# Optimization experiments

Measured on AMD Instinct MI355X. Metric: run time of the kernel, lower is better.

Reference implementation:

```python
import jax, jax.numpy as jnp
import numpy as np

DELTA_V = 0.1
DELTA_D = 0.5
NUM_LABELS = 33  # label 0 = background, instance ids 1..32


def setup_inputs() -> dict:
    key = jax.random.key(0)
    k1, k2 = jax.random.split(key)
    B, N, D = 8, 131072, 32
    embeddings = jax.random.normal(k1, (B, N, D), dtype=jnp.float32)
    labels = jax.random.randint(k2, (B, N), 0, NUM_LABELS, dtype=jnp.int32)
    return {"embeddings": embeddings, "labels": labels}


def reference(embeddings, labels):
    # embeddings: [B, N, D], labels: [B, N] int (0 = ignore)
    B = embeddings.shape[0]
    dt = embeddings.dtype

    oh = jax.nn.one_hot(labels, NUM_LABELS, dtype=dt)              # [B, N, L]
    counts = oh.sum(1)                                              # [B, L]
    sums = jnp.einsum('bnl,bnd->bld', oh, embeddings)               # [B, L, D]
    means = sums / jnp.maximum(counts, 1.0)[..., None]              # [B, L, D]

    # ---- pull loss: hinge on distance of each point to its instance mean ----
    mean_pt = jnp.take_along_axis(means, labels[..., None], axis=1)  # [B, N, D]
    diff = embeddings - mean_pt
    dist = jnp.sqrt(jnp.sum(diff * diff, -1) + 1e-24)               # [B, N]
    hinge = jnp.maximum(dist - DELTA_V, 0.0)
    seg_mean = jnp.einsum('bnl,bn->bl', oh, hinge) / jnp.maximum(counts, 1.0)  # [B, L]

    present = counts[:, 1:] > 0                                     # [B, L-1]
    n_inst = present.sum(-1).astype(dt)                             # [B]
    pull_b = seg_mean[:, 1:].sum(-1) / (n_inst + 1e-6)
    pull = pull_b.sum() / B

    # ---- push loss: hinge margin between normalized instance means ----
    m = means[:, 1:, :]                                             # [B, L-1, D]
    mn = m / jnp.maximum(jnp.linalg.norm(m, axis=-1, keepdims=True), 1e-12)
    sq = jnp.sum((mn[:, :, None, :] - mn[:, None, :, :]) ** 2, -1)  # [B, K, K]
    dmat = jnp.sqrt(sq + 1e-24)
    K = NUM_LABELS - 1
    triu = jnp.triu(jnp.ones((K, K), dt), 1)
    pmask = triu[None] * present[:, :, None].astype(dt) * present[:, None, :].astype(dt)
    hp = jnp.maximum(2.0 * DELTA_D - dmat, 0.0) * pmask
    push_b = jnp.where(n_inst > 1, hp.sum((-2, -1)) / (pmask.sum((-2, -1)) + 1e-6), 0.0)
    push = push_b.sum() / B

    total = pull + push
    return jnp.stack([total, pull, push])
```

## Files before the change

### kernel.cpp

```cpp
#include <hip/hip_runtime.h>
#include <hip/hip_bf16.h>

#define BATCH 8
#define NPTS  131072
#define DIM   32
#define NLAB  33
#define G1X   256
#define P1PTS 512
#define BPB2  128

#define OFF_CNT   0
#define OFF_SUM   264
#define OFF_PULL  (264 + 8448)
#define WS_FLOATS (OFF_PULL + BATCH * BPB2)

typedef short  bf16x8 __attribute__((ext_vector_type(8)));
typedef float  f32x4  __attribute__((ext_vector_type(4)));

static __device__ __forceinline__ short f2bf(float f) {
  __hip_bfloat16 h = __float2bfloat16(f);
  return *reinterpret_cast<short*>(&h);
}

__global__ __launch_bounds__(256) void pass1_kernel(
    const float* __restrict__ emb, const int* __restrict__ lab,
    float* __restrict__ gsum, float* __restrict__ gcnt) {
  const int b    = blockIdx.y;
  const int tid  = threadIdx.x;
  const int w    = tid >> 6;
  const int lane = tid & 63;

  constexpr int STEPS = P1PTS / 128;

  __shared__ float s_stage[4][32 * 33];
  __shared__ int   s_cnt4[4][NLAB];
  float* st = s_stage[w];

  const size_t base = (size_t)b * NPTS + (size_t)blockIdx.x * P1PTS
                    + (size_t)w * (P1PTS / 4);

  const int m0 = lane & 15;
  const int g  = lane >> 4;
  f32x4 acc[3][2];
#pragma unroll
  for (int t = 0; t < 3; ++t)
#pragma unroll
    for (int u = 0; u < 2; ++u) acc[t][u] = (f32x4){0.f, 0.f, 0.f, 0.f};
  int cnt0 = 0, cnt1 = 0, cnt2 = 0;

  float4 ld[4];
  int labv;
  {
    const float4* src = (const float4*)(emb + base * DIM);
#pragma unroll
    for (int r = 0; r < 4; ++r) ld[r] = src[lane + 64 * r];
    labv = lab[base + (lane & 31)];
  }

  for (int step = 0; step < STEPS; ++step) {
#pragma unroll
    for (int r = 0; r < 4; ++r) {
      const int i = lane + 64 * r;
      const int p = i >> 3, d0 = (i & 7) * 4;
      st[(d0 + 0) * 33 + p] = ld[r].x;
      st[(d0 + 1) * 33 + p] = ld[r].y;
      st[(d0 + 2) * 33 + p] = ld[r].z;
      st[(d0 + 3) * 33 + p] = ld[r].w;
    }
    const int labv_c = labv;

    if (step < STEPS - 1) {
      const float4* src = (const float4*)(emb + (base + (step + 1) * 32) * DIM);
#pragma unroll
      for (int r = 0; r < 4; ++r) ld[r] = src[lane + 64 * r];
      labv = lab[base + (step + 1) * 32 + (lane & 31)];
    }

    bf16x8 a0, a1, a2;
#pragma unroll
    for (int j = 0; j < 8; ++j) {
      const int lj = __shfl(labv_c, g * 8 + j);
      const int h0 = (lj == m0), h1 = (lj == m0 + 16), h2 = (lj == m0 + 32);
      a0[j] = h0 ? (short)0x3F80 : (short)0;
      a1[j] = h1 ? (short)0x3F80 : (short)0;
      a2[j] = h2 ? (short)0x3F80 : (short)0;
      cnt0 += h0; cnt1 += h1; cnt2 += h2;
    }

    bf16x8 b0, b1;
#pragma unroll
    for (int j = 0; j < 8; ++j) {
      b0[j] = f2bf(st[m0 * 33 + g * 8 + j]);
      b1[j] = f2bf(st[(m0 + 16) * 33 + g * 8 + j]);
    }

    acc[0][0] = __builtin_amdgcn_mfma_f32_16x16x32_bf16(a0, b0, acc[0][0], 0, 0, 0);
    acc[0][1] = __builtin_amdgcn_mfma_f32_16x16x32_bf16(a0, b1, acc[0][1], 0, 0, 0);
    acc[1][0] = __builtin_amdgcn_mfma_f32_16x16x32_bf16(a1, b0, acc[1][0], 0, 0, 0);
    acc[1][1] = __builtin_amdgcn_mfma_f32_16x16x32_bf16(a1, b1, acc[1][1], 0, 0, 0);
    acc[2][0] = __builtin_amdgcn_mfma_f32_16x16x32_bf16(a2, b0, acc[2][0], 0, 0, 0);
    acc[2][1] = __builtin_amdgcn_mfma_f32_16x16x32_bf16(a2, b1, acc[2][1], 0, 0, 0);
  }

  cnt0 += __shfl_xor(cnt0, 16); cnt0 += __shfl_xor(cnt0, 32);
  cnt1 += __shfl_xor(cnt1, 16); cnt1 += __shfl_xor(cnt1, 32);
  cnt2 += __shfl_xor(cnt2, 16); cnt2 += __shfl_xor(cnt2, 32);
  if (lane < 16)            s_cnt4[w][m0]      = cnt0;
  else if (lane < 32)       s_cnt4[w][m0 + 16] = cnt1;
  if (lane == 32)           s_cnt4[w][32]      = cnt2;

#pragma unroll
  for (int t = 0; t < 2; ++t)
#pragma unroll
    for (int u = 0; u < 2; ++u)
#pragma unroll
      for (int r = 0; r < 4; ++r)
        st[(t * 16 + g * 4 + r) * DIM + m0 + 16 * u] = acc[t][u][r];
  if (lane < 16) {
    st[32 * DIM + m0]      = acc[2][0][0];
    st[32 * DIM + m0 + 16] = acc[2][1][0];
  }
  __syncthreads();

  for (int i = tid; i < NLAB * DIM; i += 256) {
    const float v = s_stage[0][i] + s_stage[1][i] + s_stage[2][i] + s_stage[3][i];
    atomicAdd(&gsum[(size_t)b * (NLAB * DIM) + i], v);
  }
  if (tid < NLAB) {
    const int c = s_cnt4[0][tid] + s_cnt4[1][tid] + s_cnt4[2][tid] + s_cnt4[3][tid];
    atomicAdd(&gcnt[b * NLAB + tid], (float)c);
  }
}

#define CN 8
#define P2_ISSUE(LB, EB, C)                                                   \
  {                                                                           \
    _Pragma("unroll")                                                         \
    for (int j = 0; j < CN; ++j) {                                            \
      const size_t it = (size_t)(C) * CN + j;                                 \
      const unsigned long long al =                                           \
          (unsigned long long)(lab + base + p0 + it * PSTRIDE);               \
      asm volatile("global_load_dword %0, %1, off" : "=&v"(LB[j]) : "v"(al)); \
    }                                                                         \
    _Pragma("unroll")                                                         \
    for (int j = 0; j < CN; ++j) {                                            \
      const size_t it = (size_t)(C) * CN + j;                                 \
      const unsigned long long ae =                                           \
          (unsigned long long)(emb + (base + p0 + it * PSTRIDE) * DIM + d0);  \
      asm volatile("global_load_dwordx4 %0, %1, off" : "=&v"(EB[j]) : "v"(ae)); \
    }                                                                         \
  }

#define P2_COMPUTE(LB, EB)                                                    \
  {                                                                           \
    float s[CN];                                                              \
    _Pragma("unroll")                                                         \
    for (int j = 0; j < CN; ++j) {                                            \
      const f32x4 mv = *(const f32x4*)(s_mean + LB[j] * 36 + d0);             \
      const float dx = EB[j][0] - mv[0], dy = EB[j][1] - mv[1];               \
      const float dz = EB[j][2] - mv[2], dw = EB[j][3] - mv[3];               \
      s[j] = dx * dx + dy * dy + dz * dz + dw * dw;                           \
    }                                                                         \
    _Pragma("unroll")                                                         \
    for (int j = 0; j < CN; ++j) {                                            \
      s[j] += __shfl_xor(s[j], 1);                                            \
      s[j] += __shfl_xor(s[j], 2);                                            \
      s[j] += __shfl_xor(s[j], 4);                                            \
    }                                                                         \
    float sv = s[0];                                                          \
    int   lv = LB[0];                                                         \
    _Pragma("unroll")                                                         \
    for (int j = 1; j < CN; ++j) {                                            \
      sv = (lane8 == j) ? s[j] : sv;                                          \
      lv = (lane8 == j) ? LB[j] : lv;                                         \
    }                                                                         \
    const float dist = sqrtf(sv + 1e-24f);                                    \
    wacc += s_w[lv] * fmaxf(dist - 0.1f, 0.f);                                \
  }

__global__ __launch_bounds__(256, 4) void pass2_kernel(
    const float* __restrict__ emb, const int* __restrict__ lab,
    const float* __restrict__ gsum, const float* __restrict__ gcnt,
    float* __restrict__ pull_part) {
  const int b   = blockIdx.y;
  const int tid = threadIdx.x;
  __shared__ __align__(16) float s_mean[NLAB * 36];
  __shared__ float s_w[NLAB];
  __shared__ float s_red[4];

  for (int i = tid; i < NLAB * DIM; i += 256) {
    const int l = i >> 5, d = i & 31;
    const float c = gcnt[b * NLAB + l];
    s_mean[l * 36 + d] = gsum[b * (NLAB * DIM) + i] / fmaxf(c, 1.0f);
  }
  if (tid < 64) {
    const float c = (tid < NLAB) ? gcnt[b * NLAB + tid] : 0.f;
    const int pres = (tid >= 1 && tid < NLAB && c > 0.f) ? 1 : 0;
    const unsigned long long bal = __ballot(pres);
    const float n_inst = (float)__popcll(bal);
    if (tid < NLAB)
      s_w[tid] = pres ? 1.f / (fmaxf(c, 1.f) * (n_inst + 1e-6f)) : 0.f;
  }
  __syncthreads();

  const int sub   = tid >> 3;
  const int lane8 = tid & 7;
  const int d0    = lane8 << 2;
  const size_t base = (size_t)b * NPTS;
  const int p0 = blockIdx.x * 32 + sub;
  constexpr int PSTRIDE = BPB2 * 32;
  constexpr int NIT     = NPTS / PSTRIDE;
  constexpr int NCH     = NIT / CN;

  int   labsA[CN], labsB[CN];
  f32x4 eA[CN], eB[CN];
  float wacc = 0.f;

  P2_ISSUE(labsA, eA, 0);
#pragma unroll
  for (int cc = 0; cc < NCH; cc += 2) {
    if (cc + 1 < NCH) P2_ISSUE(labsB, eB, cc + 1);
    if (cc + 1 < NCH) { asm volatile("s_waitcnt vmcnt(16)" ::: "memory"); }
    else              { asm volatile("s_waitcnt vmcnt(0)"  ::: "memory"); }
    __builtin_amdgcn_sched_barrier(0);
    P2_COMPUTE(labsA, eA);
    if (cc + 1 < NCH) {
      if (cc + 2 < NCH) P2_ISSUE(labsA, eA, cc + 2);
      if (cc + 2 < NCH) { asm volatile("s_waitcnt vmcnt(16)" ::: "memory"); }
      else              { asm volatile("s_waitcnt vmcnt(0)"  ::: "memory"); }
      __builtin_amdgcn_sched_barrier(0);
      P2_COMPUTE(labsB, eB);
    }
  }

#pragma unroll
  for (int mm = 1; mm < 64; mm <<= 1) wacc += __shfl_xor(wacc, mm);
  if ((tid & 63) == 0) s_red[tid >> 6] = wacc;
  __syncthreads();
  if (tid == 0)
    pull_part[b * BPB2 + blockIdx.x] =
        s_red[0] + s_red[1] + s_red[2] + s_red[3];
}

__global__ __launch_bounds__(512) void finish_kernel(
    const float* __restrict__ gsum, const float* __restrict__ gcnt,
    const float* __restrict__ pull_part, float* __restrict__ out) {
  const int tid = threadIdx.x;
  const int b   = tid >> 6;
  const int t   = tid & 63;
  __shared__ __align__(16) float s_mn[BATCH * 32 * DIM];
  __shared__ float s_ps[BATCH];
  __shared__ float s_pl[BATCH];
  float* mn = s_mn + b * 32 * DIM;

  {
    float plsum = pull_part[b * BPB2 + t] + pull_part[b * BPB2 + 64 + t];
#pragma unroll
    for (int m = 1; m < 64; m <<= 1) plsum += __shfl_xor(plsum, m);
    if (t == 0) s_pl[b] = plsum;
  }

  int pres = 0;
  if (t < 32) {
    const int l = t + 1;
    const float cnt = gcnt[b * NLAB + l];
    pres = (cnt > 0.f) ? 1 : 0;
    const float inv = 1.f / fmaxf(cnt, 1.f);
    float v[DIM];
    float n2 = 0.f;
    for (int d = 0; d < DIM; d++) {
      v[d] = gsum[b * (NLAB * DIM) + l * DIM + d] * inv;
      n2  += v[d] * v[d];
    }
    const float scale = 1.f / fmaxf(sqrtf(n2), 1e-12f);
    for (int d = 0; d < DIM; d++) mn[t * DIM + d] = v[d] * scale;
  }
  const unsigned long long bal = __ballot(pres);
  const unsigned int pmask32 = (unsigned int)(bal & 0xFFFFFFFFull);
  const int n_inst = __popc(pmask32);

  __syncthreads();

  float hp_sum = 0.f, pm_sum = 0.f;
  for (int idx = t; idx < 1024; idx += 64) {
    const int i = idx >> 5, j = idx & 31;
    if (j > i && ((pmask32 >> i) & 1u) && ((pmask32 >> j) & 1u)) {
      const float4* a = (const float4*)(mn + i * DIM);
      const float4* c = (const float4*)(mn + j * DIM);
      float sq = 0.f;
      for (int q = 0; q < 8; q++) {
        const float4 av = a[q], cv = c[q];
        const float dx = av.x - cv.x, dy = av.y - cv.y;
        const float dz = av.z - cv.z, dw = av.w - cv.w;
        sq += dx * dx + dy * dy + dz * dz + dw * dw;
      }
      const float dmat = sqrtf(sq + 1e-24f);
      hp_sum += fmaxf(1.0f - dmat, 0.f);
      pm_sum += 1.f;
    }
  }
  for (int m = 1; m < 64; m <<= 1) {
    hp_sum += __shfl_xor(hp_sum, m);
    pm_sum += __shfl_xor(pm_sum, m);
  }
  const float push = (n_inst > 1) ? hp_sum / (pm_sum + 1e-6f) : 0.f;
  if (t == 0) s_ps[b] = push;
  __syncthreads();

  if (tid < 64) {
    float pl = (t < BATCH) ? s_pl[t] : 0.f;
    float ps = (t < BATCH) ? s_ps[t] : 0.f;
#pragma unroll
    for (int m = 1; m < 64; m <<= 1) {
      pl += __shfl_xor(pl, m);
      ps += __shfl_xor(ps, m);
    }
    if (t == 0) {
      const float pull_m = pl / (float)BATCH;
      const float push_m = ps / (float)BATCH;
      out[0] = pull_m + push_m;
      out[1] = pull_m;
      out[2] = push_m;
    }
  }
}

extern "C" void kernel_launch(void* const* d_in, const int* in_sizes, int n_in,
                              void* d_out, int out_size, void* d_ws, size_t ws_size,
                              hipStream_t stream) {
  const float* emb = (const float*)d_in[0];
  const int*   lab = (const int*)d_in[1];
  float* out = (float*)d_out;
  float* ws  = (float*)d_ws;

  float* gcnt  = ws + OFF_CNT;
  float* gsum  = ws + OFF_SUM;
  float* pullp = ws + OFF_PULL;

  hipMemsetAsync(d_ws, 0, WS_FLOATS * sizeof(float), stream);

  dim3 grid1(G1X, BATCH);
  dim3 grid2(BPB2, BATCH);
  pass1_kernel<<<grid1, 256, 0, stream>>>(emb, lab, gsum, gcnt);
  pass2_kernel<<<grid2, 256, 0, stream>>>(emb, lab, gsum, gcnt, pullp);
  finish_kernel<<<1, 512, 0, stream>>>(gsum, gcnt, pullp, out);
}
```

Before: 240.2 us.

## Replace pass1 global atomics with per-block partials and a separate reduce kernel

Pass1 blocks now write their per-block label sums and counts to a workspace partial buffer instead of issuing global atomicAdds. A new reduce kernel sums those partials in 8 slices and does far fewer atomics into the global sums. This removes contention from 256 blocks per batch hitting the same 1056 addresses. The cost is an extra kernel launch and about 8.6 MB of partial writes and reads.

```diff
diff --git a/kernel.cpp b/kernel.cpp
--- a/kernel.cpp
+++ b/kernel.cpp
@@ -12,7 +12,9 @@
 #define OFF_CNT   0
 #define OFF_SUM   264
 #define OFF_PULL  (264 + 8448)
-#define WS_FLOATS (OFF_PULL + BATCH * BPB2)
+#define OFF_PSUM  (OFF_PULL + BATCH * BPB2)
+#define OFF_PCNT  (OFF_PSUM + BATCH * G1X * NLAB * DIM)
+#define WS_FLOATS (OFF_PCNT + BATCH * G1X * NLAB)
 
 typedef short  bf16x8 __attribute__((ext_vector_type(8)));
 typedef float  f32x4  __attribute__((ext_vector_type(4)));
@@ -24,7 +26,7 @@
 
 __global__ __launch_bounds__(256) void pass1_kernel(
     const float* __restrict__ emb, const int* __restrict__ lab,
-    float* __restrict__ gsum, float* __restrict__ gcnt) {
+    float* __restrict__ psum, float* __restrict__ pcnt) {
   const int b    = blockIdx.y;
   const int tid  = threadIdx.x;
   const int w    = tid >> 6;
@@ -122,13 +124,44 @@
   }
   __syncthreads();
 
+  const size_t pb = (size_t)b * G1X + blockIdx.x;
   for (int i = tid; i < NLAB * DIM; i += 256) {
     const float v = s_stage[0][i] + s_stage[1][i] + s_stage[2][i] + s_stage[3][i];
-    atomicAdd(&gsum[(size_t)b * (NLAB * DIM) + i], v);
+    psum[pb * (NLAB * DIM) + i] = v;
   }
   if (tid < NLAB) {
     const int c = s_cnt4[0][tid] + s_cnt4[1][tid] + s_cnt4[2][tid] + s_cnt4[3][tid];
-    atomicAdd(&gcnt[b * NLAB + tid], (float)c);
+    pcnt[pb * NLAB + tid] = (float)c;
+  }
+}
+
+__global__ __launch_bounds__(256) void reduce_kernel(
+    const float* __restrict__ psum, const float* __restrict__ pcnt,
+    float* __restrict__ gsum, float* __restrict__ gcnt) {
+  constexpr int TOT = BATCH * NLAB * DIM;
+  constexpr int KS  = G1X / 8;
+  const int slice = blockIdx.y;
+  const int o = blockIdx.x * 256 + threadIdx.x;
+  if (o < TOT) {
+    const int b = o / (NLAB * DIM), i = o - b * (NLAB * DIM);
+    const float* src = psum + ((size_t)b * G1X + slice * KS) * (NLAB * DIM) + i;
+    float a0 = 0.f, a1 = 0.f, a2 = 0.f, a3 = 0.f;
+#pragma unroll
+    for (int k = 0; k < KS; k += 4) {
+      a0 += src[(size_t)(k + 0) * (NLAB * DIM)];
+      a1 += src[(size_t)(k + 1) * (NLAB * DIM)];
+      a2 += src[(size_t)(k + 2) * (NLAB * DIM)];
+      a3 += src[(size_t)(k + 3) * (NLAB * DIM)];
+    }
+    atomicAdd(&gsum[o], (a0 + a1) + (a2 + a3));
+  } else if (o - TOT < BATCH * NLAB) {
+    const int o2 = o - TOT;
+    const int b = o2 / NLAB, l = o2 - b * NLAB;
+    const float* src = pcnt + ((size_t)b * G1X + slice * KS) * NLAB + l;
+    float a = 0.f;
+#pragma unroll
+    for (int k = 0; k < KS; ++k) a += src[(size_t)k * NLAB];
+    atomicAdd(&gcnt[o2], a);
   }
 }
 
@@ -336,12 +369,16 @@
   float* gcnt  = ws + OFF_CNT;
   float* gsum  = ws + OFF_SUM;
   float* pullp = ws + OFF_PULL;
-
-  hipMemsetAsync(d_ws, 0, WS_FLOATS * sizeof(float), stream);
+  float* psum  = ws + OFF_PSUM;
+  float* pcnt  = ws + OFF_PCNT;
+
+  hipMemsetAsync(d_ws, 0, (OFF_SUM + BATCH * NLAB * DIM) * sizeof(float), stream);
 
   dim3 grid1(G1X, BATCH);
+  dim3 gridR((BATCH * NLAB * DIM + BATCH * NLAB + 255) / 256, 8);
   dim3 grid2(BPB2, BATCH);
-  pass1_kernel<<<grid1, 256, 0, stream>>>(emb, lab, gsum, gcnt);
+  pass1_kernel<<<grid1, 256, 0, stream>>>(emb, lab, psum, pcnt);
+  reduce_kernel<<<gridR, 256, 0, stream>>>(psum, pcnt, gsum, gcnt);
   pass2_kernel<<<grid2, 256, 0, stream>>>(emb, lab, gsum, gcnt, pullp);
   finish_kernel<<<1, 512, 0, stream>>>(gsum, gcnt, pullp, out);
 }
```

After: 237.1 us. No clear change (-1.3%).
